# Kernel optimization log

Measured on AMD Instinct MI355X. Metric: run time of the kernel, lower is better.

The kernel has to match this reference:

```python
import jax, jax.numpy as jnp
import numpy as np

N = 100_000      # nodes
E = 3_200_000    # directed edges
F_IN = 128       # node feature dim
H = 16           # hidden channels


def setup_inputs() -> dict:
    key = jax.random.key(0)
    k0, k1, k2, k3, k4, k5 = jax.random.split(key, 6)
    x = jax.random.normal(k0, (N, F_IN), dtype=jnp.float32)
    edge_index = jax.random.randint(k1, (2, E), 0, N, dtype=jnp.int32)
    W1 = jax.random.normal(k2, (F_IN, H), dtype=jnp.float32) * (1.0 / np.sqrt(F_IN))
    b1 = jax.random.normal(k3, (H,), dtype=jnp.float32) * 0.02
    W2 = jax.random.normal(k4, (H, 1), dtype=jnp.float32) * (1.0 / np.sqrt(H))
    b2 = jax.random.normal(k5, (1,), dtype=jnp.float32) * 0.02
    return {"x": x, "edge_index": edge_index, "W1": W1, "b1": b1, "W2": W2, "b2": b2}


def _gcn_conv(x, src, dst, deg_inv_sqrt, W, b):
    # PyG GCNConv: h = x @ W; out_i = sum_{j->i} norm_ij * h_j + b
    # norm_ij = deg_i^-1/2 * deg_j^-1/2 (degrees include self-loops)
    n = x.shape[0]
    h = x @ W                                   # [N, out]
    norm = deg_inv_sqrt[src] * deg_inv_sqrt[dst]  # [E+N]
    msg = h[src] * norm[:, None]                # gather + scale
    out = jax.ops.segment_sum(msg, dst, num_segments=n)
    return out + b


def reference(x, edge_index, W1, b1, W2, b2):
    n = x.shape[0]
    loops = jnp.arange(n, dtype=edge_index.dtype)
    src = jnp.concatenate([edge_index[0], loops])  # self-loops appended
    dst = jnp.concatenate([edge_index[1], loops])
    # degree of destination nodes (with self-loops), shared by both layers
    deg = jax.ops.segment_sum(jnp.ones_like(dst, dtype=x.dtype), dst, num_segments=n)
    deg_inv_sqrt = jax.lax.rsqrt(jnp.maximum(deg, 1.0))  # deg >= 1 due to self-loops

    h = jax.nn.relu(_gcn_conv(x, src, dst, deg_inv_sqrt, W1, b1))
    out = _gcn_conv(h, src, dst, deg_inv_sqrt, W2, b2)
    return out
```

## Files before the change

### kernel.cpp

```cpp
#include <hip/hip_runtime.h>
#include <hip/hip_fp16.h>

#define FIN 128
#define HC 16
#define NBLK 512
#define NB 391
#define BKT 256
#define SLOT 17408
#define SENT 0xFFFFFFFFu
#define STRIDE 80

typedef _Float16 half8 __attribute__((ext_vector_type(8)));
typedef float f32x4 __attribute__((ext_vector_type(4)));

__global__ __launch_bounds__(1024) void count_kernel(const int* __restrict__ dst,
                                                     int* __restrict__ cntTab, int E) {
    __shared__ int cnt[NB];
    int blk = blockIdx.x, t = threadIdx.x;
    for (int i = t; i < NB; i += 1024) cnt[i] = 0;
    __syncthreads();
    int slice = (((E + NBLK - 1) / NBLK) + 3) & ~3;
    int s = blk * slice, e = min(E, s + slice);
    if (s < e) {
        int n4 = (e - s) >> 2;
        const int4* d4 = (const int4*)(dst + s);
        for (int i = t; i < n4; i += 1024) {
            int4 dd = d4[i];
            atomicAdd(&cnt[dd.x >> 8], 1);
            atomicAdd(&cnt[dd.y >> 8], 1);
            atomicAdd(&cnt[dd.z >> 8], 1);
            atomicAdd(&cnt[dd.w >> 8], 1);
        }
    }
    __syncthreads();
    for (int i = t; i < NB; i += 1024) cntTab[i * NBLK + blk] = cnt[i];
}

__global__ void rowscan_kernel(const int* __restrict__ cntTab, int* __restrict__ rowEx,
                               int* __restrict__ bucketTotal) {
    __shared__ int wsum[8];
    int b = blockIdx.x, t = threadIdx.x;
    int own = cntTab[b * NBLK + t];
    int rnd = (own + 15) & ~15;
    int sc = rnd;
#pragma unroll
    for (int off = 1; off < 64; off <<= 1) {
        int v = __shfl_up(sc, off);
        if ((t & 63) >= off) sc += v;
    }
    if ((t & 63) == 63) wsum[t >> 6] = sc;
    __syncthreads();
    int pre = 0;
#pragma unroll
    for (int w = 0; w < 8; ++w)
        if (w < (t >> 6)) pre += wsum[w];
    int inc = sc + pre;
    rowEx[b * NBLK + t] = inc - rnd;
    if (t == NBLK - 1) bucketTotal[b] = inc;
}

__global__ __launch_bounds__(1024) void scatter_kernel(const int* __restrict__ src,
                                                       const int* __restrict__ dst,
                                                       const int* __restrict__ rowEx,
                                                       unsigned int* __restrict__ ebuf, int E) {
    __shared__ int base[NB];
    __shared__ int cur[NB];
    int blk = blockIdx.x, t = threadIdx.x;
    for (int i = t; i < NB; i += 1024) {
        base[i] = i * SLOT + rowEx[i * NBLK + blk];
        cur[i] = 0;
    }
    __syncthreads();
    int slice = (((E + NBLK - 1) / NBLK) + 3) & ~3;
    int s = blk * slice, e = min(E, s + slice);
    if (s < e) {
        int n4 = (e - s) >> 2;
        const int4* d4 = (const int4*)(dst + s);
        const int4* s4 = (const int4*)(src + s);
        for (int i = t; i < n4; i += 1024) {
            int4 dd = d4[i];
            int4 ss = s4[i];
            int b0 = dd.x >> 8, p0 = atomicAdd(&cur[b0], 1);
            ebuf[base[b0] + p0] = ((unsigned)ss.x << 8) | (unsigned)(dd.x & 255);
            int b1 = dd.y >> 8, p1 = atomicAdd(&cur[b1], 1);
            ebuf[base[b1] + p1] = ((unsigned)ss.y << 8) | (unsigned)(dd.y & 255);
            int b2 = dd.z >> 8, p2 = atomicAdd(&cur[b2], 1);
            ebuf[base[b2] + p2] = ((unsigned)ss.z << 8) | (unsigned)(dd.z & 255);
            int b3 = dd.w >> 8, p3 = atomicAdd(&cur[b3], 1);
            ebuf[base[b3] + p3] = ((unsigned)ss.w << 8) | (unsigned)(dd.w & 255);
        }
    }
    __syncthreads();
    for (int i = t; i < NB; i += 1024) {
        int c = cur[i], r = (c + 15) & ~15;
        int bb = base[i];
        for (int p = c; p < r; ++p) ebuf[bb + p] = SENT;
    }
}

__global__ __launch_bounds__(1024) void sortdis_kernel(const unsigned int* __restrict__ ebuf,
                                                       const int* __restrict__ bucketTotal,
                                                       int* __restrict__ csr, int* __restrict__ deg,
                                                       float* __restrict__ dis, int n) {
    __shared__ int cnt[BKT];
    int b = blockIdx.x, t = threadIdx.x;
    if (t < BKT) cnt[t] = 0;
    __syncthreads();
    int s0 = b * SLOT;
    int total = bucketTotal[b];
    int n4 = total >> 2;
    const uint4* e4 = (const uint4*)(ebuf + s0);
    size_t cbase = (size_t)b * BKT * STRIDE;
    for (int idx = t; idx < n4; idx += 1024) {
        uint4 u = e4[idx];
        if (u.x != SENT) { int l = u.x & 255; int r = atomicAdd(&cnt[l], 1); csr[cbase + l * STRIDE + r] = (int)(u.x >> 8); }
        if (u.y != SENT) { int l = u.y & 255; int r = atomicAdd(&cnt[l], 1); csr[cbase + l * STRIDE + r] = (int)(u.y >> 8); }
        if (u.z != SENT) { int l = u.z & 255; int r = atomicAdd(&cnt[l], 1); csr[cbase + l * STRIDE + r] = (int)(u.z >> 8); }
        if (u.w != SENT) { int l = u.w & 255; int r = atomicAdd(&cnt[l], 1); csr[cbase + l * STRIDE + r] = (int)(u.w >> 8); }
    }
    __syncthreads();
    if (t < BKT) {
        int node = b * BKT + t;
        if (node < n) {
            deg[node] = cnt[t];
            dis[node] = rsqrtf((float)cnt[t] + 1.0f);
        }
    }
}

__global__ void h1_mfma_kernel(const float* __restrict__ x, const float* __restrict__ W1,
                               const float* __restrict__ dis, __half* __restrict__ hs16, int n) {
    __shared__ float xs[64][132];
    int t = threadIdx.x;
    int wave = t >> 6;
    int lane = t & 63;
    int r = lane & 15, g = lane >> 4;
    int rowbase0 = blockIdx.x * 64;
#pragma unroll
    for (int it = 0; it < 8; ++it) {
        int i = it * 256 + t;
        int row = i >> 5, c4 = i & 31;
        int grow = rowbase0 + row;
        const float4* xr = (const float4*)(x + (size_t)(grow < n ? grow : n - 1) * FIN);
        float4 v = xr[c4];
        xs[row][c4 * 4 + 0] = v.x;
        xs[row][c4 * 4 + 1] = v.y;
        xs[row][c4 * 4 + 2] = v.z;
        xs[row][c4 * 4 + 3] = v.w;
    }
    half8 bfrag[4];
#pragma unroll
    for (int i = 0; i < 4; ++i)
#pragma unroll
        for (int j = 0; j < 8; ++j)
            bfrag[i][j] = (_Float16)W1[(i * 32 + g * 8 + j) * HC + r];
    __syncthreads();
    int rowbase = wave * 16;
    f32x4 acc = {0.f, 0.f, 0.f, 0.f};
#pragma unroll
    for (int i = 0; i < 4; ++i) {
        const float4* rowp = (const float4*)&xs[rowbase + r][i * 32 + g * 8];
        float4 v0 = rowp[0];
        float4 v1 = rowp[1];
        half8 afrag;
        afrag[0] = (_Float16)v0.x; afrag[1] = (_Float16)v0.y;
        afrag[2] = (_Float16)v0.z; afrag[3] = (_Float16)v0.w;
        afrag[4] = (_Float16)v1.x; afrag[5] = (_Float16)v1.y;
        afrag[6] = (_Float16)v1.z; afrag[7] = (_Float16)v1.w;
        acc = __builtin_amdgcn_mfma_f32_16x16x32_f16(afrag, bfrag[i], acc, 0, 0, 0);
    }
#pragma unroll
    for (int j = 0; j < 4; ++j) {
        int orow = rowbase0 + rowbase + g * 4 + j;
        if (orow < n) hs16[(size_t)orow * HC + r] = __float2half(acc[j] * dis[orow]);
    }
}

#define GSTEP(T)                                                            \
    {                                                                       \
        int e_ = (T) * 8 + eg;                                              \
        int s_ = __shfl(sidx, e_);                                          \
        float2 f_ = __half22float2(hs16[(size_t)s_ * 8 + cp]);              \
        if (e_ < mm) { ax += f_.x; ay += f_.y; }                            \
    }

__global__ void pull_layer1_kernel(const int* __restrict__ deg, const int* __restrict__ csr,
                                   const __half2* __restrict__ hs16,
                                   const float* __restrict__ b1, const float* __restrict__ W2,
                                   float* __restrict__ h2s, int n) {
    int node = (blockIdx.x * blockDim.x + threadIdx.x) >> 6;
    if (node >= n) return;
    int lane = threadIdx.x & 63;
    int cp = lane & 7;
    int eg = lane >> 3;
    int start = node * STRIDE;
    int c = csr[start + lane];
    int m = deg[node];
    int sidx = (lane < m) ? c : 0;
    int mm = min(m, 64);
    float ax = 0.f, ay = 0.f;
    if (mm <= 32) {
        GSTEP(0) GSTEP(1) GSTEP(2) GSTEP(3)
    } else if (mm <= 48) {
        GSTEP(0) GSTEP(1) GSTEP(2) GSTEP(3) GSTEP(4) GSTEP(5)
    } else {
        GSTEP(0) GSTEP(1) GSTEP(2) GSTEP(3) GSTEP(4) GSTEP(5) GSTEP(6) GSTEP(7)
        for (int k = 64 + eg; k < m; k += 8) {
            float2 f = __half22float2(hs16[(size_t)csr[start + k] * 8 + cp]);
            ax += f.x; ay += f.y;
        }
    }
    ax += __shfl_xor(ax, 8);  ay += __shfl_xor(ay, 8);
    ax += __shfl_xor(ax, 16); ay += __shfl_xor(ay, 16);
    ax += __shfl_xor(ax, 32); ay += __shfl_xor(ay, 32);
    float d = rsqrtf((float)m + 1.0f);
    float2 self = __half22float2(hs16[(size_t)node * 8 + cp]);
    float h1a = fmaxf(fmaf(d, ax + self.x, b1[2 * cp]), 0.f);
    float h1b = fmaxf(fmaf(d, ay + self.y, b1[2 * cp + 1]), 0.f);
    float v = h1a * W2[2 * cp] + h1b * W2[2 * cp + 1];
    v += __shfl_xor(v, 1);
    v += __shfl_xor(v, 2);
    v += __shfl_xor(v, 4);
    if (lane == 0) h2s[node] = v * d;
}

__global__ void pull_layer2_kernel(const int* __restrict__ deg, const int* __restrict__ csr,
                                   const float* __restrict__ h2s,
                                   const float* __restrict__ b2, float* __restrict__ out, int n) {
    int g = blockIdx.x * blockDim.x + threadIdx.x;
    int node = g >> 3;
    if (node >= n) return;
    int q = g & 7;
    int start = node * STRIDE;
    int m = deg[node];
    float a = 0.f;
    int k = q;
    for (; k + 24 < m; k += 32) {
        int i0 = csr[start + k];
        int i1 = csr[start + k + 8];
        int i2 = csr[start + k + 16];
        int i3 = csr[start + k + 24];
        float g0 = h2s[i0], g1 = h2s[i1], g2 = h2s[i2], g3 = h2s[i3];
        a += (g0 + g1) + (g2 + g3);
    }
    for (; k < m; k += 8) a += h2s[csr[start + k]];
    a += __shfl_xor(a, 1);
    a += __shfl_xor(a, 2);
    a += __shfl_xor(a, 4);
    if (q == 0) out[node] = rsqrtf((float)m + 1.0f) * (a + h2s[node]) + b2[0];
}

extern "C" void kernel_launch(void* const* d_in, const int* in_sizes, int n_in,
                              void* d_out, int out_size, void* d_ws, size_t ws_size,
                              hipStream_t stream) {
    const float* x  = (const float*)d_in[0];
    const int* ei   = (const int*)d_in[1];
    const float* W1 = (const float*)d_in[2];
    const float* b1 = (const float*)d_in[3];
    const float* W2 = (const float*)d_in[4];
    const float* b2 = (const float*)d_in[5];
    float* out = (float*)d_out;

    const int n = in_sizes[0] / FIN;
    const int E = in_sizes[1] / 2;
    const int* src = ei;
    const int* dst = ei + E;

    const size_t EB = (size_t)NB * SLOT;
    unsigned int* ebuf = (unsigned int*)d_ws;
    int* csr           = (int*)(ebuf + EB);
    int* cntTab        = csr + (size_t)100000 * STRIDE + 128;
    int* rowEx         = cntTab + NB * NBLK;
    int* bucketTotal   = rowEx + NB * NBLK;
    int* deg           = bucketTotal + 392;
    float* dis         = (float*)(deg + n);
    float* h2s         = dis + n;
    __half* hs16       = (__half*)(h2s + n);

    count_kernel<<<NBLK, 1024, 0, stream>>>(dst, cntTab, E);
    rowscan_kernel<<<NB, NBLK, 0, stream>>>(cntTab, rowEx, bucketTotal);
    scatter_kernel<<<NBLK, 1024, 0, stream>>>(src, dst, rowEx, ebuf, E);
    sortdis_kernel<<<NB, 1024, 0, stream>>>(ebuf, bucketTotal, csr, deg, dis, n);
    h1_mfma_kernel<<<(n + 63) / 64, 256, 0, stream>>>(x, W1, dis, hs16, n);
    pull_layer1_kernel<<<(n * 64 + 511) / 512, 512, 0, stream>>>(deg, csr, (const __half2*)hs16, b1, W2, h2s, n);
    pull_layer2_kernel<<<(n * 8 + 255) / 256, 256, 0, stream>>>(deg, csr, h2s, b2, out, n);
}
```

Before: 111.6 us.

## Process two nodes per wavefront in layer-1 pull and widen layer-2 gather

The layer-1 aggregation kernel now handles two destination nodes per 64-lane wavefront, interleaving their gather steps so more independent loads are in flight and per-wave overhead (csr/deg loads, reductions, bias/weight loads) is amortized. The layer-2 kernel uses 16 lanes per node instead of 8 with a shallower unroll and larger blocks. It assumes n is even (int2 deg load, n1 = n0+1 without a bounds check), which holds for the fixed problem size.

Measured after the change: 107.7 us. -3.5%, faster.

```diff
diff --git a/kernel.cpp b/kernel.cpp
--- a/kernel.cpp
+++ b/kernel.cpp
@@ -176,77 +176,99 @@
     }
 }
 
-#define GSTEP(T)                                                            \
+#define GSTEP2(T, SIDX, MM, AX, AY)                                         \
     {                                                                       \
         int e_ = (T) * 8 + eg;                                              \
-        int s_ = __shfl(sidx, e_);                                          \
+        int s_ = __shfl((SIDX), e_);                                        \
         float2 f_ = __half22float2(hs16[(size_t)s_ * 8 + cp]);              \
-        if (e_ < mm) { ax += f_.x; ay += f_.y; }                            \
+        if (e_ < (MM)) { (AX) += f_.x; (AY) += f_.y; }                      \
     }
 
 __global__ void pull_layer1_kernel(const int* __restrict__ deg, const int* __restrict__ csr,
                                    const __half2* __restrict__ hs16,
                                    const float* __restrict__ b1, const float* __restrict__ W2,
                                    float* __restrict__ h2s, int n) {
-    int node = (blockIdx.x * blockDim.x + threadIdx.x) >> 6;
-    if (node >= n) return;
+    int wid = (blockIdx.x * blockDim.x + threadIdx.x) >> 6;
+    int n0 = wid * 2;
+    if (n0 >= n) return;
+    int n1 = n0 + 1;
     int lane = threadIdx.x & 63;
     int cp = lane & 7;
     int eg = lane >> 3;
-    int start = node * STRIDE;
-    int c = csr[start + lane];
-    int m = deg[node];
-    int sidx = (lane < m) ? c : 0;
-    int mm = min(m, 64);
-    float ax = 0.f, ay = 0.f;
-    if (mm <= 32) {
-        GSTEP(0) GSTEP(1) GSTEP(2) GSTEP(3)
-    } else if (mm <= 48) {
-        GSTEP(0) GSTEP(1) GSTEP(2) GSTEP(3) GSTEP(4) GSTEP(5)
-    } else {
-        GSTEP(0) GSTEP(1) GSTEP(2) GSTEP(3) GSTEP(4) GSTEP(5) GSTEP(6) GSTEP(7)
-        for (int k = 64 + eg; k < m; k += 8) {
-            float2 f = __half22float2(hs16[(size_t)csr[start + k] * 8 + cp]);
-            ax += f.x; ay += f.y;
-        }
-    }
-    ax += __shfl_xor(ax, 8);  ay += __shfl_xor(ay, 8);
-    ax += __shfl_xor(ax, 16); ay += __shfl_xor(ay, 16);
-    ax += __shfl_xor(ax, 32); ay += __shfl_xor(ay, 32);
-    float d = rsqrtf((float)m + 1.0f);
-    float2 self = __half22float2(hs16[(size_t)node * 8 + cp]);
-    float h1a = fmaxf(fmaf(d, ax + self.x, b1[2 * cp]), 0.f);
-    float h1b = fmaxf(fmaf(d, ay + self.y, b1[2 * cp + 1]), 0.f);
-    float v = h1a * W2[2 * cp] + h1b * W2[2 * cp + 1];
-    v += __shfl_xor(v, 1);
-    v += __shfl_xor(v, 2);
-    v += __shfl_xor(v, 4);
-    if (lane == 0) h2s[node] = v * d;
+    int p0 = csr[n0 * STRIDE + lane];
+    int p1 = csr[n1 * STRIDE + lane];
+    int2 mpair = ((const int2*)deg)[wid];
+    int m0 = mpair.x, m1 = mpair.y;
+    int c0 = (lane < m0) ? p0 : 0;
+    int c1 = (lane < m1) ? p1 : 0;
+    int mm0 = min(m0, 64), mm1 = min(m1, 64);
+    float ax0 = 0.f, ay0 = 0.f, ax1 = 0.f, ay1 = 0.f;
+    GSTEP2(0, c0, mm0, ax0, ay0) GSTEP2(0, c1, mm1, ax1, ay1)
+    GSTEP2(1, c0, mm0, ax0, ay0) GSTEP2(1, c1, mm1, ax1, ay1)
+    GSTEP2(2, c0, mm0, ax0, ay0) GSTEP2(2, c1, mm1, ax1, ay1)
+    GSTEP2(3, c0, mm0, ax0, ay0) GSTEP2(3, c1, mm1, ax1, ay1)
+    if (mm0 > 32) {
+        GSTEP2(4, c0, mm0, ax0, ay0) GSTEP2(5, c0, mm0, ax0, ay0)
+        GSTEP2(6, c0, mm0, ax0, ay0) GSTEP2(7, c0, mm0, ax0, ay0)
+        for (int k = 64 + eg; k < m0; k += 8) {
+            float2 f = __half22float2(hs16[(size_t)csr[n0 * STRIDE + k] * 8 + cp]);
+            ax0 += f.x; ay0 += f.y;
+        }
+    }
+    if (mm1 > 32) {
+        GSTEP2(4, c1, mm1, ax1, ay1) GSTEP2(5, c1, mm1, ax1, ay1)
+        GSTEP2(6, c1, mm1, ax1, ay1) GSTEP2(7, c1, mm1, ax1, ay1)
+        for (int k = 64 + eg; k < m1; k += 8) {
+            float2 f = __half22float2(hs16[(size_t)csr[n1 * STRIDE + k] * 8 + cp]);
+            ax1 += f.x; ay1 += f.y;
+        }
+    }
+    ax0 += __shfl_xor(ax0, 8);  ay0 += __shfl_xor(ay0, 8);
+    ax1 += __shfl_xor(ax1, 8);  ay1 += __shfl_xor(ay1, 8);
+    ax0 += __shfl_xor(ax0, 16); ay0 += __shfl_xor(ay0, 16);
+    ax1 += __shfl_xor(ax1, 16); ay1 += __shfl_xor(ay1, 16);
+    ax0 += __shfl_xor(ax0, 32); ay0 += __shfl_xor(ay0, 32);
+    ax1 += __shfl_xor(ax1, 32); ay1 += __shfl_xor(ay1, 32);
+    float2 self0 = __half22float2(hs16[(size_t)n0 * 8 + cp]);
+    float2 self1 = __half22float2(hs16[(size_t)n1 * 8 + cp]);
+    float bb = b1[2 * cp], bb2 = b1[2 * cp + 1];
+    float w = W2[2 * cp], w2 = W2[2 * cp + 1];
+    float d0 = rsqrtf((float)m0 + 1.0f);
+    float d1 = rsqrtf((float)m1 + 1.0f);
+    float v0 = fmaxf(fmaf(d0, ax0 + self0.x, bb), 0.f) * w
+             + fmaxf(fmaf(d0, ay0 + self0.y, bb2), 0.f) * w2;
+    float v1 = fmaxf(fmaf(d1, ax1 + self1.x, bb), 0.f) * w
+             + fmaxf(fmaf(d1, ay1 + self1.y, bb2), 0.f) * w2;
+    v0 += __shfl_xor(v0, 1); v1 += __shfl_xor(v1, 1);
+    v0 += __shfl_xor(v0, 2); v1 += __shfl_xor(v1, 2);
+    v0 += __shfl_xor(v0, 4); v1 += __shfl_xor(v1, 4);
+    if (lane == 0) {
+        h2s[n0] = v0 * d0;
+        h2s[n1] = v1 * d1;
+    }
 }
 
 __global__ void pull_layer2_kernel(const int* __restrict__ deg, const int* __restrict__ csr,
                                    const float* __restrict__ h2s,
                                    const float* __restrict__ b2, float* __restrict__ out, int n) {
     int g = blockIdx.x * blockDim.x + threadIdx.x;
-    int node = g >> 3;
+    int node = g >> 4;
     if (node >= n) return;
-    int q = g & 7;
+    int q = g & 15;
     int start = node * STRIDE;
     int m = deg[node];
     float a = 0.f;
     int k = q;
-    for (; k + 24 < m; k += 32) {
+    for (; k + 16 < m; k += 32) {
         int i0 = csr[start + k];
-        int i1 = csr[start + k + 8];
-        int i2 = csr[start + k + 16];
-        int i3 = csr[start + k + 24];
-        float g0 = h2s[i0], g1 = h2s[i1], g2 = h2s[i2], g3 = h2s[i3];
-        a += (g0 + g1) + (g2 + g3);
-    }
-    for (; k < m; k += 8) a += h2s[csr[start + k]];
+        int i1 = csr[start + k + 16];
+        a += h2s[i0] + h2s[i1];
+    }
+    for (; k < m; k += 16) a += h2s[csr[start + k]];
     a += __shfl_xor(a, 1);
     a += __shfl_xor(a, 2);
     a += __shfl_xor(a, 4);
+    a += __shfl_xor(a, 8);
     if (q == 0) out[node] = rsqrtf((float)m + 1.0f) * (a + h2s[node]) + b2[0];
 }
 
@@ -282,6 +304,6 @@
     scatter_kernel<<<NBLK, 1024, 0, stream>>>(src, dst, rowEx, ebuf, E);
     sortdis_kernel<<<NB, 1024, 0, stream>>>(ebuf, bucketTotal, csr, deg, dis, n);
     h1_mfma_kernel<<<(n + 63) / 64, 256, 0, stream>>>(x, W1, dis, hs16, n);
-    pull_layer1_kernel<<<(n * 64 + 511) / 512, 512, 0, stream>>>(deg, csr, (const __half2*)hs16, b1, W2, h2s, n);
-    pull_layer2_kernel<<<(n * 8 + 255) / 256, 256, 0, stream>>>(deg, csr, h2s, b2, out, n);
-}
+    pull_layer1_kernel<<<(n / 2 * 64 + 511) / 512, 512, 0, stream>>>(deg, csr, (const __half2*)hs16, b1, W2, h2s, n);
+    pull_layer2_kernel<<<(n * 16 + 511) / 512, 512, 0, stream>>>(deg, csr, h2s, b2, out, n);
+}
```
